# Performance work log

Hardware: AMD Instinct MI355X
Metric: run time of the kernel (lower is better)

The kernel has to match this reference:

```python
import jax, jax.numpy as jnp
import numpy as np
from jax import lax

EPS = 1e-5
K = 13  # correlation window (pad 6 each side)

def _conv(x, w, b):
    # 3x3 conv, stride 1, padding 1, NCHW/OIHW
    y = lax.conv_general_dilated(x, w, (1, 1), ((1, 1), (1, 1)),
                                 dimension_numbers=('NCHW', 'OIHW', 'NCHW'))
    return y + b[None, :, None, None]

def _inorm(x):
    # InstanceNorm2d: per-sample per-channel, biased var, no affine
    m = jnp.mean(x, axis=(2, 3), keepdims=True)
    v = jnp.mean((x - m) ** 2, axis=(2, 3), keepdims=True)
    return (x - m) * lax.rsqrt(v + EPS)

def _block(x, wa, ba, wb, bb):
    x = jax.nn.relu(_conv(x, wa, ba))
    x = jax.nn.relu(_conv(x, wb, bb))
    return _inorm(x)

def _forward(color, corr, w1a, b1a, w1b, b1b, w2a, b2a, w2b, b2b,
             w3a, b3a, w3b, b3b, w4a, b4a, w4b, b4b, H, W):
    conv1 = _block(color[:, :, ::2, ::2], w1a, b1a, w1b, b1b)   # (B,64,2H,2W)
    conv2 = _block(conv1[:, :, ::2, ::2], w2a, b2a, w2b, b2b)   # (B,128,H,W)
    B, C = conv2.shape[0], conv2.shape[1]
    pad = jnp.pad(conv2, ((0, 0), (0, 0), (6, 6), (6, 6)), mode='edge')
    # 'pre' mode: content-adaptive 13x13 windowed weighted sum.
    # accumulating corr[:, t] * shifted-window of conv2_pad.
    def body(acc, t):
        i, j = t // K, t % K
        patch = lax.dynamic_slice(pad, (0, 0, i, j), (B, C, H, W))
        acc = acc + corr[:, t][:, None, :] * patch.reshape(B, C, H * W)
        return acc, None
    align, _ = lax.scan(body, jnp.zeros((B, C, H * W), conv2.dtype),
                        jnp.arange(K * K))
    align_1 = align.reshape(B, C, H, W)                          # (B,128,H,W)
    align_2 = _block(align_1[:, :, ::2, ::2], w3a, b3a, w3b, b3b)  # (B,256,H/2,W/2)
    align_3 = _block(align_2[:, :, ::2, ::2], w4a, b4a, w4b, b4b)  # (B,512,H/4,W/4)
    return (align_1, align_2, align_3)

def setup_inputs() -> dict:
    key = jax.random.key(0)
    ks = jax.random.split(key, 20)
    def w(k, shape):
        return jax.random.normal(k, shape, jnp.float32) * 0.05
    B, H, W = 4, 128, 128
    inp = {
        'color': jax.random.normal(ks[0], (B, 2, 4 * H, 4 * W), jnp.float32),
        'corr': jax.random.normal(ks[1], (B, K * K, H * W), jnp.float32) * 0.05,
        'w1a': w(ks[2], (64, 2, 3, 3)),    'b1a': jnp.zeros((64,), jnp.float32),
        'w1b': w(ks[3], (64, 64, 3, 3)),   'b1b': jnp.zeros((64,), jnp.float32),
        'w2a': w(ks[4], (128, 64, 3, 3)),  'b2a': jnp.zeros((128,), jnp.float32),
        'w2b': w(ks[5], (128, 128, 3, 3)), 'b2b': jnp.zeros((128,), jnp.float32),
        'w3a': w(ks[6], (256, 128, 3, 3)), 'b3a': jnp.zeros((256,), jnp.float32),
        'w3b': w(ks[7], (256, 256, 3, 3)), 'b3b': jnp.zeros((256,), jnp.float32),
        'w4a': w(ks[8], (512, 256, 3, 3)), 'b4a': jnp.zeros((512,), jnp.float32),
        'w4b': w(ks[9], (512, 512, 3, 3)), 'b4b': jnp.zeros((512,), jnp.float32),
        'H': H, 'W': W,
    }
    return inp

def reference(color, corr, w1a, b1a, w1b, b1b, w2a, b2a, w2b, b2b,
              w3a, b3a, w3b, b3b, w4a, b4a, w4b, b4b, H, W):
    return _forward(color, corr, w1a, b1a, w1b, b1b, w2a, b2a, w2b, b2b,
                    w3a, b3a, w3b, b3b, w4a, b4a, w4b, b4b, H, W)
```

## Files before the change

kernel.cpp:

```cpp
#include <hip/hip_runtime.h>
#include <hip/hip_bf16.h>

typedef __hip_bfloat16 bf16;
typedef __attribute__((ext_vector_type(8))) short short8;
typedef __attribute__((ext_vector_type(4))) float f32x4;
typedef __attribute__((address_space(1))) const void gas_void;
typedef __attribute__((address_space(3))) void las_void;

__device__ __forceinline__ float b2f(bf16 v) { return __bfloat162float(v); }
__device__ __forceinline__ bf16 f2b(float v) { return __float2bfloat16(v); }
__device__ __forceinline__ short fbits(float v) {
  bf16 h = f2b(v); return *reinterpret_cast<short*>(&h);
}
__device__ __forceinline__ float sb2f(short s) {
  return b2f(*reinterpret_cast<bf16*>(&s));
}
__device__ __forceinline__ int xcd_swz(int bid, int nwg) {
  int q = nwg >> 3, r = nwg & 7;
  int xcd = bid & 7, idx = bid >> 3;
  return (xcd < r ? xcd * (q + 1) : r * (q + 1) + (xcd - r) * q) + idx;
}

struct RDesc {
  const float* w[7];
  int off8[7];
  int cin[7], cout[7];
  int base[8];
};

__global__ __launch_bounds__(256) void repack_all_k(RDesc d, short* __restrict__ Wr,
                                                    float* __restrict__ zerop)
{
  if (blockIdx.x == 0 && threadIdx.x < 16) zerop[threadIdx.x] = 0.f;
  int blk = blockIdx.x;
  int l = 0;
  while (l < 6 && blk >= d.base[l + 1]) ++l;
  const int Cin = d.cin[l], Cout = d.cout[l];
  const int nkc = Cin >> 5, ncof = Cout >> 4;
  const size_t gid = (size_t)(blk - d.base[l]) * 256 + threadIdx.x;
  const int lane = gid & 63;
  size_t r = gid >> 6;
  const int tap = r % 9; r /= 9;
  const int kcc = r % nkc; r /= nkc;
  const int cof = r % ncof;
  const int hl = r / ncof;
  const float* w = d.w[l];
  const int co = cof * 16 + (lane & 15);
  short8 v;
#pragma unroll
  for (int j = 0; j < 8; ++j) {
    int ci = kcc * 32 + ((lane >> 4) * 8 + j);
    float wv = w[((size_t)co * Cin + ci) * 9 + tap];
    bf16 hi = f2b(wv);
    v[j] = hl ? fbits(wv - b2f(hi)) : *reinterpret_cast<short*>(&hi);
  }
  *reinterpret_cast<short8*>(Wr + ((size_t)d.off8[l] + gid) * 8) = v;
}

template<int R, int CX, int S, int LO, int GL>
__global__ __launch_bounds__(256) void conv_mfma_k(
    const bf16* __restrict__ src, bf16* __restrict__ dst,
    const short8* __restrict__ Wr, const float* __restrict__ bias,
    const float2* __restrict__ stats, float* __restrict__ pout,
    const float* __restrict__ zerop,
    int Win, int Hout, int Wout, int Cin, int Cout, int XT, int KS)
{
  constexpr int ROWS = R + 2;
  constexpr int COLS = CX + 2;
  constexpr int NGR = ROWS * 4 * COLS;
  constexpr int FM = (R * CX) / 32;
  __shared__ short8 a_s[NGR];

  const int ytn = Hout / R;
  const int nxy = XT * ytn;
  const int ncog = Cout >> 6;
  const int wg = xcd_swz(blockIdx.x, gridDim.x);
  const int ks = wg / (ncog * 4 * nxy);
  const int rem2 = wg - ks * (ncog * 4 * nxy);
  const int cog = rem2 / (4 * nxy);
  const int rem = rem2 - cog * (4 * nxy);
  const int b = rem / nxy;
  const int pxb = rem - b * nxy;
  const int xt = pxb % XT, yt = pxb / XT;
  const int x0 = xt * CX, y0 = yt * R;

  const int tid = threadIdx.x, lane = tid & 63, wid = tid >> 6;
  const int wm = wid & 1, wn = wid >> 1;
  const int nkc = Cin >> 5;
  const int nkcs = nkc / KS;
  const int kc0 = ks * nkcs;
  const int ncof = Cout >> 4;
  const int l15 = lane & 15, lg = lane >> 4;

  f32x4 acc[FM][2] = {};

  int arow[FM], acolb[FM];
#pragma unroll
  for (int fm = 0; fm < FM; ++fm) {
    int p = wm * (R * CX / 2) + fm * 16 + l15;
    arow[fm] = p / CX;
    acolb[fm] = p % CX;
  }

  auto bload = [&](int hl, int fn, int kcc, int tap) -> short8 {
    int cof = cog * 4 + wn * 2 + fn;
    return Wr[((((size_t)hl * ncof + cof) * nkc + kcc) * 9 + tap) * 64 + lane];
  };

  short8 bc[2][2], bn_[2][2];
  bc[0][0] = bload(0, 0, kc0, 0); bc[0][1] = bload(0, 1, kc0, 0);
  if (LO) { bc[1][0] = bload(1, 0, kc0, 0); bc[1][1] = bload(1, 1, kc0, 0); }

  for (int kc = kc0; kc < kc0 + nkcs; ++kc) {
    __syncthreads();
    if (GL) {
      for (int s = tid; s < NGR; s += 256) {
        int col = s % COLS, rg = s / COLS;
        int row = rg >> 2, g = rg & 3;
        int sy = y0 + row - 1;
        int sx = x0 + col - 1;
        const short* gp;
        if (sy >= 0 && sy < Hout && sx >= 0 && sx < Wout) {
          int ry = S ? 2 * sy : sy, rx = S ? 2 * sx : sx;
          gp = reinterpret_cast<const short*>(src) +
               (((size_t)b * (S ? 2 * Hout : Hout) + ry) * Win + rx) * Cin +
               kc * 32 + g * 8;
        } else {
          gp = reinterpret_cast<const short*>(zerop);
        }
        __builtin_amdgcn_global_load_lds((gas_void*)gp, (las_void*)&a_s[s], 16, 0, 0);
      }
    } else {
      for (int idx = tid; idx < NGR; idx += 256) {
        int g = idx & 3, cix = idx >> 2;
        int col = cix % COLS, row = cix / COLS;
        int sy = y0 + row - 1;
        int sx = x0 + col - 1;
        short8 v = {};
        if (sy >= 0 && sy < Hout && sx >= 0 && sx < Wout) {
          int ry = S ? 2 * sy : sy, rx = S ? 2 * sx : sx;
          v = *reinterpret_cast<const short8*>(
              reinterpret_cast<const short*>(src) +
              (((size_t)b * (S ? 2 * Hout : Hout) + ry) * Win + rx) * Cin +
              kc * 32 + g * 8);
          if (stats) {
            const float2* st = stats + (size_t)b * Cin + kc * 32 + g * 8;
#pragma unroll
            for (int j = 0; j < 8; ++j)
              v[j] = fbits((sb2f(v[j]) - st[j].x) * st[j].y);
          }
        }
        a_s[(row * 4 + g) * COLS + col] = v;
      }
    }
    __syncthreads();

#pragma unroll
    for (int tap = 0; tap < 9; ++tap) {
      const int dy = tap / 3, dx = tap % 3;
      int nt = tap + 1, nk = kc;
      if (nt == 9) { nt = 0; nk = (kc + 1 < kc0 + nkcs) ? kc + 1 : kc0; }
      bn_[0][0] = bload(0, 0, nk, nt); bn_[0][1] = bload(0, 1, nk, nt);
      if (LO) { bn_[1][0] = bload(1, 0, nk, nt); bn_[1][1] = bload(1, 1, nk, nt); }
      if (LO) {
#pragma unroll
        for (int fm = 0; fm < FM; fm += 2) {
          short8 a0 = a_s[((arow[fm] + dy) * 4 + lg) * COLS + acolb[fm] + dx];
          short8 a1 = a_s[((arow[fm + 1] + dy) * 4 + lg) * COLS + acolb[fm + 1] + dx];
          acc[fm][0]     = __builtin_amdgcn_mfma_f32_16x16x32_bf16(a0, bc[0][0], acc[fm][0], 0, 0, 0);
          acc[fm + 1][0] = __builtin_amdgcn_mfma_f32_16x16x32_bf16(a1, bc[0][0], acc[fm + 1][0], 0, 0, 0);
          acc[fm][1]     = __builtin_amdgcn_mfma_f32_16x16x32_bf16(a0, bc[0][1], acc[fm][1], 0, 0, 0);
          acc[fm + 1][1] = __builtin_amdgcn_mfma_f32_16x16x32_bf16(a1, bc[0][1], acc[fm + 1][1], 0, 0, 0);
          acc[fm][0]     = __builtin_amdgcn_mfma_f32_16x16x32_bf16(a0, bc[1][0], acc[fm][0], 0, 0, 0);
          acc[fm + 1][0] = __builtin_amdgcn_mfma_f32_16x16x32_bf16(a1, bc[1][0], acc[fm + 1][0], 0, 0, 0);
          acc[fm][1]     = __builtin_amdgcn_mfma_f32_16x16x32_bf16(a0, bc[1][1], acc[fm][1], 0, 0, 0);
          acc[fm + 1][1] = __builtin_amdgcn_mfma_f32_16x16x32_bf16(a1, bc[1][1], acc[fm + 1][1], 0, 0, 0);
        }
      } else {
#pragma unroll
        for (int fm = 0; fm < FM; ++fm) {
          short8 a = a_s[((arow[fm] + dy) * 4 + lg) * COLS + acolb[fm] + dx];
          acc[fm][0] = __builtin_amdgcn_mfma_f32_16x16x32_bf16(a, bc[0][0], acc[fm][0], 0, 0, 0);
          acc[fm][1] = __builtin_amdgcn_mfma_f32_16x16x32_bf16(a, bc[0][1], acc[fm][1], 0, 0, 0);
        }
      }
      bc[0][0] = bn_[0][0]; bc[0][1] = bn_[0][1];
      if (LO) { bc[1][0] = bn_[1][0]; bc[1][1] = bn_[1][1]; }
    }
  }

#pragma unroll
  for (int fn = 0; fn < 2; ++fn) {
    int co = cog * 64 + wn * 32 + fn * 16 + l15;
    float bs = bias[co];
#pragma unroll
    for (int fm = 0; fm < FM; ++fm) {
#pragma unroll
      for (int j = 0; j < 4; ++j) {
        int p = wm * (R * CX / 2) + fm * 16 + lg * 4 + j;
        int r = p / CX, x = p % CX;
        size_t oi = ((size_t)(b * Hout + y0 + r) * Wout + x0 + x) * Cout + co;
        if (pout) {
          pout[(size_t)ks * ((size_t)4 * Hout * Wout * Cout) + oi] = acc[fm][fn][j];
        } else {
          dst[oi] = f2b(fmaxf(acc[fm][fn][j] + bs, 0.f));
        }
      }
    }
  }
}

__global__ __launch_bounds__(256) void combine2_k(
    const float* __restrict__ p, const float* __restrict__ bias,
    bf16* __restrict__ dst, int n4, int Cout)
{
  int i = blockIdx.x * 256 + threadIdx.x;
  if (i >= n4) return;
  float4 a = reinterpret_cast<const float4*>(p)[i];
  float4 c = reinterpret_cast<const float4*>(p + (size_t)n4 * 4)[i];
  int co = (i * 4) & (Cout - 1);
  float4 bs = *reinterpret_cast<const float4*>(bias + co);
  short v0 = fbits(fmaxf(a.x + c.x + bs.x, 0.f));
  short v1 = fbits(fmaxf(a.y + c.y + bs.y, 0.f));
  short v2 = fbits(fmaxf(a.z + c.z + bs.z, 0.f));
  short v3 = fbits(fmaxf(a.w + c.w + bs.w, 0.f));
  short4 pk = make_short4(v0, v1, v2, v3);
  *reinterpret_cast<short4*>(reinterpret_cast<short*>(dst) + (size_t)i * 4) = pk;
}

__global__ __launch_bounds__(256) void conv1a_k(
    const float* __restrict__ src, bf16* __restrict__ dst,
    const float* __restrict__ w, const float* __restrict__ bias)
{
  const int b = blockIdx.z, cog = blockIdx.y;
  const int ty0 = (blockIdx.x / 16) * 16, tx0 = (blockIdx.x % 16) * 16;
  const int tid = threadIdx.x, tx = tid & 15, ty = tid >> 4;

  __shared__ float in_s[2][18][18];
  __shared__ __align__(16) float w_s[2][3][3][16];

  for (int idx = tid; idx < 2 * 324; idx += 256) {
    int ci = idx / 324, r = idx - ci * 324;
    int iy = r / 18, ix = r - iy * 18;
    int gy = ty0 + iy - 1, gx = tx0 + ix - 1;
    float v = 0.f;
    if (gy >= 0 && gy < 256 && gx >= 0 && gx < 256)
      v = src[((size_t)(b * 2 + ci) * 512 + 2 * gy) * 512 + 2 * gx];
    in_s[ci][iy][ix] = v;
  }
  for (int idx = tid; idx < 2 * 144; idx += 256) {
    int co = idx & 15, r = idx >> 4;
    int ci = r / 9, k = r - ci * 9;
    w_s[ci][k / 3][k % 3][co] = w[(size_t)((cog * 16 + co) * 2 + ci) * 9 + k];
  }
  __syncthreads();

  float acc[16];
#pragma unroll
  for (int i = 0; i < 16; ++i) acc[i] = 0.f;
  for (int ci = 0; ci < 2; ++ci)
#pragma unroll
    for (int dy = 0; dy < 3; ++dy)
#pragma unroll
      for (int dx = 0; dx < 3; ++dx) {
        float v = in_s[ci][ty + dy][tx + dx];
        const float4* wv = (const float4*)(&w_s[ci][dy][dx][0]);
        float4 w0 = wv[0], w1 = wv[1], w2 = wv[2], w3 = wv[3];
        acc[0] = fmaf(v, w0.x, acc[0]);   acc[1] = fmaf(v, w0.y, acc[1]);
        acc[2] = fmaf(v, w0.z, acc[2]);   acc[3] = fmaf(v, w0.w, acc[3]);
        acc[4] = fmaf(v, w1.x, acc[4]);   acc[5] = fmaf(v, w1.y, acc[5]);
        acc[6] = fmaf(v, w1.z, acc[6]);   acc[7] = fmaf(v, w1.w, acc[7]);
        acc[8] = fmaf(v, w2.x, acc[8]);   acc[9] = fmaf(v, w2.y, acc[9]);
        acc[10] = fmaf(v, w2.z, acc[10]); acc[11] = fmaf(v, w2.w, acc[11]);
        acc[12] = fmaf(v, w3.x, acc[12]); acc[13] = fmaf(v, w3.y, acc[13]);
        acc[14] = fmaf(v, w3.z, acc[14]); acc[15] = fmaf(v, w3.w, acc[15]);
      }

  const int gy = ty0 + ty, gx = tx0 + tx;
  short8 s0, s1;
#pragma unroll
  for (int j = 0; j < 8; ++j) {
    s0[j] = fbits(fmaxf(acc[j] + bias[cog * 16 + j], 0.f));
    s1[j] = fbits(fmaxf(acc[8 + j] + bias[cog * 16 + 8 + j], 0.f));
  }
  short8* dp = reinterpret_cast<short8*>(
      reinterpret_cast<short*>(dst) + (((size_t)(b * 256 + gy) * 256 + gx) * 64 + cog * 16));
  dp[0] = s0; dp[1] = s1;
}

__global__ __launch_bounds__(256) void inorm_stats1_k(
    const bf16* __restrict__ x, float2* __restrict__ part,
    int HW, int C, int nb, int PC)
{
  const int b = blockIdx.y, pc = blockIdx.x;
  const int NC8 = C >> 3;
  const int pgc = 256 / NC8;
  const int c8 = (threadIdx.x % NC8) * 8;
  const int pg = threadIdx.x / NC8;
  const int chunk = HW / PC;
  const int p0 = pc * chunk;

  float s[8] = {}, ss[8] = {};
  for (int p = p0 + pg; p < p0 + chunk; p += pgc) {
    short8 v = *reinterpret_cast<const short8*>(
        reinterpret_cast<const short*>(x) + ((size_t)b * HW + p) * C + c8);
#pragma unroll
    for (int j = 0; j < 8; ++j) {
      float f = sb2f(v[j]);
      s[j] += f; ss[j] += f * f;
    }
  }
  __shared__ float sh[2][2048];
#pragma unroll
  for (int j = 0; j < 8; ++j) {
    sh[0][pg * C + c8 + j] = s[j];
    sh[1][pg * C + c8 + j] = ss[j];
  }
  __syncthreads();
  for (int c = threadIdx.x; c < C; c += 256) {
    float as = 0.f, aq = 0.f;
    for (int g = 0; g < pgc; ++g) { as += sh[0][g * C + c]; aq += sh[1][g * C + c]; }
    part[((size_t)pc * nb + b) * C + c] = make_float2(as, aq);
  }
}

__global__ __launch_bounds__(256) void inorm_stats2_k(
    const float2* __restrict__ part, float2* __restrict__ stats,
    int HW, int C, int PC, int nb)
{
  const int b = blockIdx.y, cg = blockIdx.x;
  const int c = threadIdx.x & 63, i = threadIdx.x >> 6;
  float s = 0.f, ss = 0.f;
  for (int pc = i; pc < PC; pc += 4) {
    float2 v = part[((size_t)pc * nb + b) * C + cg * 64 + c];
    s += v.x; ss += v.y;
  }
  __shared__ float sh[2][4][64];
  sh[0][i][c] = s; sh[1][i][c] = ss;
  __syncthreads();
  if (threadIdx.x < 64) {
    int cc = threadIdx.x;
    float s4 = sh[0][0][cc] + sh[0][1][cc] + sh[0][2][cc] + sh[0][3][cc];
    float q4 = sh[1][0][cc] + sh[1][1][cc] + sh[1][2][cc] + sh[1][3][cc];
    float m = s4 / (float)HW;
    float var = q4 / (float)HW - m * m;
    stats[(size_t)b * C + cg * 64 + cc] = make_float2(m, rsqrtf(var + 1e-5f));
  }
}

__global__ __launch_bounds__(256) void inorm_apply_k(
    const bf16* __restrict__ x, const float2* __restrict__ stats, int HW, int C,
    bf16* __restrict__ dnhwc, float* __restrict__ fnchw)
{
  const int b = blockIdx.z, cg = blockIdx.y;
  const int c = cg * 64 + (threadIdx.x & 63);
  const int p = blockIdx.x * 4 + (threadIdx.x >> 6);
  const float2 st = stats[(size_t)b * C + c];
  const size_t ia = ((size_t)b * HW + p) * C + c;
  const float v = (b2f(x[ia]) - st.x) * st.y;
  if (dnhwc) dnhwc[ia] = f2b(v);
  if (fnchw) fnchw[((size_t)(b * C + c)) * HW + p] = v;
}

__global__ __launch_bounds__(256) void inorm_apply_pad_k(
    const bf16* __restrict__ x, const float2* __restrict__ stats,
    bf16* __restrict__ pad)
{
  const int b = blockIdx.z, cg = blockIdx.y, yy = blockIdx.x;
  const int tid = threadIdx.x;
  __shared__ bf16 t_s[64][130];
  __shared__ float2 st_s[64];
  if (tid < 64) st_s[tid] = stats[(size_t)b * 128 + cg * 64 + tid];
  __syncthreads();

  const int c8 = (tid & 7) * 8, px0 = tid >> 3;
#pragma unroll
  for (int pass = 0; pass < 4; ++pass) {
    int px = pass * 32 + px0;
    short8 v = *reinterpret_cast<const short8*>(
        reinterpret_cast<const short*>(x) +
        ((size_t)(b * 16384 + yy * 128 + px) * 128 + cg * 64 + c8));
#pragma unroll
    for (int j = 0; j < 8; ++j) {
      float2 st = st_s[c8 + j];
      t_s[c8 + j][px] = f2b((sb2f(v[j]) - st.x) * st.y);
    }
  }
  __syncthreads();

  for (int idx = tid; idx < 64 * 18; idx += 256) {
    int c = idx / 18, g = idx - (idx / 18) * 18;
    short8 v;
#pragma unroll
    for (int j = 0; j < 8; ++j) {
      int xx = g * 8 + j - 6;
      xx = xx < 0 ? 0 : (xx > 127 ? 127 : xx);
      v[j] = *reinterpret_cast<short*>(&t_s[c][xx]);
    }
    *reinterpret_cast<short8*>(
        reinterpret_cast<short*>(pad) +
        ((size_t)(b * 128 + cg * 64 + c) * 128 + yy) * 144 + g * 8) = v;
  }
}

__global__ __launch_bounds__(256) void corr_mfma_k(
    const float* __restrict__ corr, const bf16* __restrict__ pad,
    float* __restrict__ outc, bf16* __restrict__ outn, int b0)
{
  __shared__ __align__(16) char smem[26 * 64 * 16];
  short8* a_lds = reinterpret_cast<short8*>(smem);
  float* out_s = reinterpret_cast<float*>(smem);

  const int b = b0 + blockIdx.z;
  const int wg = xcd_swz(blockIdx.x, gridDim.x);
  const int y = wg >> 3, xt = wg & 7;
  const int x0 = xt * 16;
  const int tid = threadIdx.x, lane = tid & 63, wid = tid >> 6;
  const int l15 = lane & 15, lg = lane >> 4;

  for (int idx = tid; idx < 26 * 64; idx += 256) {
    short8 z = {};
    a_lds[idx] = z;
  }
  __syncthreads();

  unsigned short* ah = reinterpret_cast<unsigned short*>(a_lds);
  for (int idx = tid; idx < 169 * 16; idx += 256) {
    int t = idx >> 4, m = idx & 15;
    int dy = t / 13, dx = t - dy * 13;
    float f = corr[((size_t)b * 169 + t) * 16384 + y * 128 + x0 + m];
    bf16 hi = f2b(f);
    unsigned short hb = *reinterpret_cast<unsigned short*>(&hi);
    unsigned short lb = (unsigned short)fbits(f - b2f(hi));
    int k = m + dx;
    int ent = dy * 64 + (k >> 3) * 16 + m;
    ah[ent * 8 + (k & 7)] = hb;
    ah[(13 * 64 + ent) * 8 + (k & 7)] = lb;
  }
  __syncthreads();

  const int cg0 = wid * 2;
  f32x4 a0h = {}, a0l = {}, a1h = {}, a1l = {};
  const short* pb = reinterpret_cast<const short*>(pad);

  for (int dy = 0; dy < 13; ++dy) {
    int rowc = y + dy - 6; rowc = rowc < 0 ? 0 : (rowc > 127 ? 127 : rowc);
    short8 bhi = a_lds[dy * 64 + lane];
    short8 blo = a_lds[(13 + dy) * 64 + lane];
    size_t base0 = ((size_t)(b * 128 + cg0 * 16 + l15) * 128 + rowc) * 144
                   + x0 + lg * 8;
    short8 a0 = *reinterpret_cast<const short8*>(pb + base0);
    short8 a1 = *reinterpret_cast<const short8*>(pb + base0 + (size_t)16 * 128 * 144);
    a0h = __builtin_amdgcn_mfma_f32_16x16x32_bf16(a0, bhi, a0h, 0, 0, 0);
    a1h = __builtin_amdgcn_mfma_f32_16x16x32_bf16(a1, bhi, a1h, 0, 0, 0);
    a0l = __builtin_amdgcn_mfma_f32_16x16x32_bf16(a0, blo, a0l, 0, 0, 0);
    a1l = __builtin_amdgcn_mfma_f32_16x16x32_bf16(a1, blo, a1l, 0, 0, 0);
  }
  f32x4 acc0 = a0h + a0l, acc1 = a1h + a1l;
  __syncthreads();

#pragma unroll
  for (int cgi = 0; cgi < 2; ++cgi) {
    f32x4 a = cgi ? acc1 : acc0;
    float* dst4 = out_s + l15 * 132 + (cg0 + cgi) * 16 + lg * 4;
    *reinterpret_cast<f32x4*>(dst4) = a;
  }
  __syncthreads();

  {
    int px_ = tid >> 4, c8 = (tid & 15) * 8;
    const float* row = out_s + px_ * 132 + c8;
    short8 v;
#pragma unroll
    for (int j = 0; j < 8; ++j) v[j] = fbits(row[j]);
    *reinterpret_cast<short8*>(
        reinterpret_cast<short*>(outn) +
        ((size_t)(b * 16384 + y * 128 + x0 + px_)) * 128 + c8) = v;
  }
  {
    int ch = tid >> 1, pg = tid & 1;
    float v0[4], v1[4];
#pragma unroll
    for (int i = 0; i < 4; ++i) v0[i] = out_s[(pg * 8 + i) * 132 + ch];
#pragma unroll
    for (int i = 0; i < 4; ++i) v1[i] = out_s[(pg * 8 + 4 + i) * 132 + ch];
    float* dst = outc + ((size_t)(b * 128 + ch)) * 16384 + y * 128 + x0 + pg * 8;
    *reinterpret_cast<float4*>(dst) = make_float4(v0[0], v0[1], v0[2], v0[3]);
    *reinterpret_cast<float4*>(dst + 4) = make_float4(v1[0], v1[1], v1[2], v1[3]);
  }
}

extern "C" void kernel_launch(void* const* d_in, const int* in_sizes, int n_in,
                              void* d_out, int out_size, void* d_ws, size_t ws_size,
                              hipStream_t stream) {
  const float* color = (const float*)d_in[0];
  const float* corr  = (const float*)d_in[1];
  const float* w1a = (const float*)d_in[2];  const float* b1a = (const float*)d_in[3];
  const float* w1b = (const float*)d_in[4];  const float* b1b = (const float*)d_in[5];
  const float* w2a = (const float*)d_in[6];  const float* b2a = (const float*)d_in[7];
  const float* w2b = (const float*)d_in[8];  const float* b2b = (const float*)d_in[9];
  const float* w3a = (const float*)d_in[10]; const float* b3a = (const float*)d_in[11];
  const float* w3b = (const float*)d_in[12]; const float* b3b = (const float*)d_in[13];
  const float* w4a = (const float*)d_in[14]; const float* b4a = (const float*)d_in[15];
  const float* w4b = (const float*)d_in[16]; const float* b4b = (const float*)d_in[17];

  float* out = (float*)d_out;
  char* ws = (char*)d_ws;
  const size_t MB = 1048576;
  float2* stats = (float2*)ws;
  short*  WrS   = (short*)(ws + (64 << 10));
  float2* part  = (float2*)(ws + 63 * MB);
  float*  zerop = (float*)(ws + 63 * MB + (800 << 10));
  bf16* P0 = (bf16*)(ws + 10 * MB);
  bf16* P1 = (bf16*)(ws + 27 * MB);
  bf16* P2 = (bf16*)(ws + 44 * MB);
  float* PK = (float*)(ws + 10 * MB);
  bf16* X1 = P0;
  bf16* X2 = (bf16*)d_out;
  const float2* nost = (const float2*)nullptr;
  float* nop = (float*)nullptr;

  RDesc rd;
  rd.w[0] = w1b; rd.w[1] = w2a; rd.w[2] = w2b; rd.w[3] = w3a;
  rd.w[4] = w3b; rd.w[5] = w4a; rd.w[6] = w4b;
  const int off8[7]  = {0, 9216, 27648, 64512, 101376, 175104, 322560};
  const int cin_[7]  = {64, 64, 128, 128, 256, 256, 512};
  const int cout_[7] = {64, 128, 128, 256, 256, 512, 512};
  int bases[8]; bases[0] = 0;
  const int nblk[7] = {36, 72, 144, 144, 288, 576, 1152};
  for (int i = 0; i < 7; ++i) { rd.off8[i] = off8[i]; rd.cin[i] = cin_[i];
    rd.cout[i] = cout_[i]; bases[i + 1] = bases[i] + nblk[i]; }
  for (int i = 0; i < 8; ++i) rd.base[i] = bases[i];
  const short8* WrV = (const short8*)WrS;

  repack_all_k<<<bases[7], 256, 0, stream>>>(rd, WrS, zerop);

  conv1a_k<<<dim3(256, 4, 4), 256, 0, stream>>>(color, X1, w1a, b1a);
  conv_mfma_k<16, 16, 0, 1, 1><<<1024, 256, 0, stream>>>(
      X1, X2, WrV + off8[0], b1b, nost, nop, zerop, 256, 256, 256, 64, 64, 16, 1);
  inorm_stats1_k<<<dim3(64, 4), 256, 0, stream>>>(X2, part, 65536, 64, 4, 64);
  inorm_stats2_k<<<dim3(1, 4), 256, 0, stream>>>(part, stats, 65536, 64, 64, 4);

  conv_mfma_k<16, 16, 1, 1, 0><<<512, 256, 0, stream>>>(
      X2, P0, WrV + off8[1], b2a, stats, nop, zerop, 256, 128, 128, 64, 128, 8, 1);
  conv_mfma_k<16, 16, 0, 1, 1><<<512, 256, 0, stream>>>(
      P0, P1, WrV + off8[2], b2b, nost, nop, zerop, 128, 128, 128, 128, 128, 8, 1);
  inorm_stats1_k<<<dim3(64, 4), 256, 0, stream>>>(P1, part, 16384, 128, 4, 64);
  inorm_stats2_k<<<dim3(2, 4), 256, 0, stream>>>(part, stats, 16384, 128, 64, 4);
  inorm_apply_pad_k<<<dim3(128, 2, 4), 256, 0, stream>>>(P1, stats, P2);

  corr_mfma_k<<<dim3(128 * 8, 1, 4), 256, 0, stream>>>(corr, P2, out, P0, 0);

  conv_mfma_k<8, 16, 1, 0, 1><<<512, 256, 0, stream>>>(
      P0, P1, WrV + off8[3], b3a, nost, nop, zerop, 128, 64, 64, 128, 256, 4, 1);
  conv_mfma_k<8, 16, 0, 0, 1><<<512, 256, 0, stream>>>(
      P1, P2, WrV + off8[4], b3b, nost, nop, zerop, 64, 64, 64, 256, 256, 4, 1);
  inorm_stats1_k<<<dim3(32, 4), 256, 0, stream>>>(P2, part, 4096, 256, 4, 32);
  inorm_stats2_k<<<dim3(4, 4), 256, 0, stream>>>(part, stats, 4096, 256, 32, 4);
  inorm_apply_k<<<dim3(1024, 4, 4), 256, 0, stream>>>(
      P2, stats, 4096, 256, (bf16*)nullptr, out + 8388608);

  conv_mfma_k<4, 16, 1, 0, 0><<<1024, 256, 0, stream>>>(
      P2, (bf16*)nullptr, WrV + off8[5], b4a, stats, PK, zerop, 64, 32, 32, 256, 512, 2, 2);
  combine2_k<<<2048, 256, 0, stream>>>(PK, b4a, P1, 524288, 512);
  conv_mfma_k<4, 16, 0, 0, 1><<<1024, 256, 0, stream>>>(
      P1, (bf16*)nullptr, WrV + off8[6], b4b, nost, PK, zerop, 32, 32, 32, 512, 512, 2, 2);
  combine2_k<<<2048, 256, 0, stream>>>(PK, b4b, P2, 524288, 512);
  inorm_stats1_k<<<dim3(32, 4), 256, 0, stream>>>(P2, part, 1024, 512, 4, 32);
  inorm_stats2_k<<<dim3(8, 4), 256, 0, stream>>>(part, stats, 1024, 512, 32, 4);
  inorm_apply_k<<<dim3(256, 8, 4), 256, 0, stream>>>(
      P2, stats, 1024, 512, (bf16*)nullptr, out + 12582912);
}
```

Before: 416.6 us.

## Reuse LDS rows across vertical taps via register strips; enable split-bf16 for level-3 convs

Adds an ST template mode that reorders the 9 taps column-major. For each horizontal offset it loads one register strip of FM+2 rows from LDS, and the three vertical taps index into that strip instead of issuing separate LDS reads. This cuts LDS read traffic per tap roughly threefold, at the cost of extra registers. The level-3 convs are also switched to LO=1 (hi/lo bf16 weight split), so their weight repack storage doubles and the workspace offsets shift; this adds MFMA work, presumably for accuracy.

Result: slower. 475.1 us (+14.0%).

```diff
diff --git a/kernel.cpp b/kernel.cpp
--- a/kernel.cpp
+++ b/kernel.cpp
@@ -57,7 +57,7 @@
   *reinterpret_cast<short8*>(Wr + ((size_t)d.off8[l] + gid) * 8) = v;
 }
 
-template<int R, int CX, int S, int LO, int GL>
+template<int R, int CX, int S, int LO, int GL, int ST>
 __global__ __launch_bounds__(256) void conv_mfma_k(
     const bf16* __restrict__ src, bf16* __restrict__ dst,
     const short8* __restrict__ Wr, const float* __restrict__ bias,
@@ -69,6 +69,7 @@
   constexpr int COLS = CX + 2;
   constexpr int NGR = ROWS * 4 * COLS;
   constexpr int FM = (R * CX) / 32;
+  static_assert(CX == 16, "strip addressing assumes CX==16");
   __shared__ short8 a_s[NGR];
 
   const int ytn = Hout / R;
@@ -110,6 +111,8 @@
   short8 bc[2][2], bn_[2][2];
   bc[0][0] = bload(0, 0, kc0, 0); bc[0][1] = bload(0, 1, kc0, 0);
   if (LO) { bc[1][0] = bload(1, 0, kc0, 0); bc[1][1] = bload(1, 1, kc0, 0); }
+
+  short8 strip[FM + 2];
 
   for (int kc = kc0; kc < kc0 + nkcs; ++kc) {
     __syncthreads();
@@ -155,37 +158,80 @@
     }
     __syncthreads();
 
-#pragma unroll
-    for (int tap = 0; tap < 9; ++tap) {
-      const int dy = tap / 3, dx = tap % 3;
-      int nt = tap + 1, nk = kc;
-      if (nt == 9) { nt = 0; nk = (kc + 1 < kc0 + nkcs) ? kc + 1 : kc0; }
-      bn_[0][0] = bload(0, 0, nk, nt); bn_[0][1] = bload(0, 1, nk, nt);
-      if (LO) { bn_[1][0] = bload(1, 0, nk, nt); bn_[1][1] = bload(1, 1, nk, nt); }
-      if (LO) {
-#pragma unroll
-        for (int fm = 0; fm < FM; fm += 2) {
-          short8 a0 = a_s[((arow[fm] + dy) * 4 + lg) * COLS + acolb[fm] + dx];
-          short8 a1 = a_s[((arow[fm + 1] + dy) * 4 + lg) * COLS + acolb[fm + 1] + dx];
-          acc[fm][0]     = __builtin_amdgcn_mfma_f32_16x16x32_bf16(a0, bc[0][0], acc[fm][0], 0, 0, 0);
-          acc[fm + 1][0] = __builtin_amdgcn_mfma_f32_16x16x32_bf16(a1, bc[0][0], acc[fm + 1][0], 0, 0, 0);
-          acc[fm][1]     = __builtin_amdgcn_mfma_f32_16x16x32_bf16(a0, bc[0][1], acc[fm][1], 0, 0, 0);
-          acc[fm + 1][1] = __builtin_amdgcn_mfma_f32_16x16x32_bf16(a1, bc[0][1], acc[fm + 1][1], 0, 0, 0);
-          acc[fm][0]     = __builtin_amdgcn_mfma_f32_16x16x32_bf16(a0, bc[1][0], acc[fm][0], 0, 0, 0);
-          acc[fm + 1][0] = __builtin_amdgcn_mfma_f32_16x16x32_bf16(a1, bc[1][0], acc[fm + 1][0], 0, 0, 0);
-          acc[fm][1]     = __builtin_amdgcn_mfma_f32_16x16x32_bf16(a0, bc[1][1], acc[fm][1], 0, 0, 0);
-          acc[fm + 1][1] = __builtin_amdgcn_mfma_f32_16x16x32_bf16(a1, bc[1][1], acc[fm + 1][1], 0, 0, 0);
+    if (ST) {
+#pragma unroll
+      for (int ti = 0; ti < 9; ++ti) {
+        const int dxM = ti / 3, dyM = ti % 3;
+        int tn = ti + 1, nk = kc, ntap;
+        if (tn == 9) { ntap = 0; nk = (kc + 1 < kc0 + nkcs) ? kc + 1 : kc0; }
+        else ntap = (tn % 3) * 3 + (tn / 3);
+        bn_[0][0] = bload(0, 0, nk, ntap); bn_[0][1] = bload(0, 1, nk, ntap);
+        if (LO) { bn_[1][0] = bload(1, 0, nk, ntap); bn_[1][1] = bload(1, 1, nk, ntap); }
+
+        if (dyM == 0) {
+#pragma unroll
+          for (int r = 0; r < FM + 2; ++r)
+            strip[r] = a_s[((wm * FM + r) * 4 + lg) * COLS + l15 + dxM];
         }
-      } else {
-#pragma unroll
-        for (int fm = 0; fm < FM; ++fm) {
-          short8 a = a_s[((arow[fm] + dy) * 4 + lg) * COLS + acolb[fm] + dx];
-          acc[fm][0] = __builtin_amdgcn_mfma_f32_16x16x32_bf16(a, bc[0][0], acc[fm][0], 0, 0, 0);
-          acc[fm][1] = __builtin_amdgcn_mfma_f32_16x16x32_bf16(a, bc[0][1], acc[fm][1], 0, 0, 0);
+
+        if (LO) {
+#pragma unroll
+          for (int fm = 0; fm < FM; fm += 2) {
+            short8 a0 = strip[fm + dyM];
+            short8 a1 = strip[fm + 1 + dyM];
+            acc[fm][0]     = __builtin_amdgcn_mfma_f32_16x16x32_bf16(a0, bc[0][0], acc[fm][0], 0, 0, 0);
+            acc[fm + 1][0] = __builtin_amdgcn_mfma_f32_16x16x32_bf16(a1, bc[0][0], acc[fm + 1][0], 0, 0, 0);
+            acc[fm][1]     = __builtin_amdgcn_mfma_f32_16x16x32_bf16(a0, bc[0][1], acc[fm][1], 0, 0, 0);
+            acc[fm + 1][1] = __builtin_amdgcn_mfma_f32_16x16x32_bf16(a1, bc[0][1], acc[fm + 1][1], 0, 0, 0);
+            acc[fm][0]     = __builtin_amdgcn_mfma_f32_16x16x32_bf16(a0, bc[1][0], acc[fm][0], 0, 0, 0);
+            acc[fm + 1][0] = __builtin_amdgcn_mfma_f32_16x16x32_bf16(a1, bc[1][0], acc[fm + 1][0], 0, 0, 0);
+            acc[fm][1]     = __builtin_amdgcn_mfma_f32_16x16x32_bf16(a0, bc[1][1], acc[fm][1], 0, 0, 0);
+            acc[fm + 1][1] = __builtin_amdgcn_mfma_f32_16x16x32_bf16(a1, bc[1][1], acc[fm + 1][1], 0, 0, 0);
+          }
+        } else {
+#pragma unroll
+          for (int fm = 0; fm < FM; ++fm) {
+            short8 a = strip[fm + dyM];
+            acc[fm][0] = __builtin_amdgcn_mfma_f32_16x16x32_bf16(a, bc[0][0], acc[fm][0], 0, 0, 0);
+            acc[fm][1] = __builtin_amdgcn_mfma_f32_16x16x32_bf16(a, bc[0][1], acc[fm][1], 0, 0, 0);
+          }
         }
+        bc[0][0] = bn_[0][0]; bc[0][1] = bn_[0][1];
+        if (LO) { bc[1][0] = bn_[1][0]; bc[1][1] = bn_[1][1]; }
       }
-      bc[0][0] = bn_[0][0]; bc[0][1] = bn_[0][1];
-      if (LO) { bc[1][0] = bn_[1][0]; bc[1][1] = bn_[1][1]; }
+    } else {
+#pragma unroll
+      for (int tap = 0; tap < 9; ++tap) {
+        const int dy = tap / 3, dx = tap % 3;
+        int nt = tap + 1, nk = kc;
+        if (nt == 9) { nt = 0; nk = (kc + 1 < kc0 + nkcs) ? kc + 1 : kc0; }
+        bn_[0][0] = bload(0, 0, nk, nt); bn_[0][1] = bload(0, 1, nk, nt);
+        if (LO) { bn_[1][0] = bload(1, 0, nk, nt); bn_[1][1] = bload(1, 1, nk, nt); }
+        if (LO) {
+#pragma unroll
+          for (int fm = 0; fm < FM; fm += 2) {
+            short8 a0 = a_s[((arow[fm] + dy) * 4 + lg) * COLS + acolb[fm] + dx];
+            short8 a1 = a_s[((arow[fm + 1] + dy) * 4 + lg) * COLS + acolb[fm + 1] + dx];
+            acc[fm][0]     = __builtin_amdgcn_mfma_f32_16x16x32_bf16(a0, bc[0][0], acc[fm][0], 0, 0, 0);
+            acc[fm + 1][0] = __builtin_amdgcn_mfma_f32_16x16x32_bf16(a1, bc[0][0], acc[fm + 1][0], 0, 0, 0);
+            acc[fm][1]     = __builtin_amdgcn_mfma_f32_16x16x32_bf16(a0, bc[0][1], acc[fm][1], 0, 0, 0);
+            acc[fm + 1][1] = __builtin_amdgcn_mfma_f32_16x16x32_bf16(a1, bc[0][1], acc[fm + 1][1], 0, 0, 0);
+            acc[fm][0]     = __builtin_amdgcn_mfma_f32_16x16x32_bf16(a0, bc[1][0], acc[fm][0], 0, 0, 0);
+            acc[fm + 1][0] = __builtin_amdgcn_mfma_f32_16x16x32_bf16(a1, bc[1][0], acc[fm + 1][0], 0, 0, 0);
+            acc[fm][1]     = __builtin_amdgcn_mfma_f32_16x16x32_bf16(a0, bc[1][1], acc[fm][1], 0, 0, 0);
+            acc[fm + 1][1] = __builtin_amdgcn_mfma_f32_16x16x32_bf16(a1, bc[1][1], acc[fm + 1][1], 0, 0, 0);
+          }
+        } else {
+#pragma unroll
+          for (int fm = 0; fm < FM; ++fm) {
+            short8 a = a_s[((arow[fm] + dy) * 4 + lg) * COLS + acolb[fm] + dx];
+            acc[fm][0] = __builtin_amdgcn_mfma_f32_16x16x32_bf16(a, bc[0][0], acc[fm][0], 0, 0, 0);
+            acc[fm][1] = __builtin_amdgcn_mfma_f32_16x16x32_bf16(a, bc[0][1], acc[fm][1], 0, 0, 0);
+          }
+        }
+        bc[0][0] = bn_[0][0]; bc[0][1] = bn_[0][1];
+        if (LO) { bc[1][0] = bn_[1][0]; bc[1][1] = bn_[1][1]; }
+      }
     }
   }
 
@@ -509,13 +555,13 @@
   const size_t MB = 1048576;
   float2* stats = (float2*)ws;
   short*  WrS   = (short*)(ws + (64 << 10));
-  float2* part  = (float2*)(ws + 63 * MB);
-  float*  zerop = (float*)(ws + 63 * MB + (800 << 10));
-  bf16* P0 = (bf16*)(ws + 10 * MB);
-  bf16* P1 = (bf16*)(ws + 27 * MB);
-  bf16* P2 = (bf16*)(ws + 44 * MB);
-  float* PK = (float*)(ws + 10 * MB);
-  bf16* X1 = P0;
+  float*  zerop = (float*)(ws + 11 * MB + (512 << 10));
+  float2* part  = (float2*)(ws + 11 * MB + (768 << 10));
+  bf16* P0 = (bf16*)(ws + 12 * MB);
+  bf16* P1 = (bf16*)(ws + 29 * MB);
+  bf16* P2 = (bf16*)(ws + 46 * MB);
+  float* PK = (float*)(ws + 12 * MB);
+  bf16* X1 = (bf16*)(ws + 29 * MB);
   bf16* X2 = (bf16*)d_out;
   const float2* nost = (const float2*)nullptr;
   float* nop = (float*)nullptr;
@@ -523,11 +569,11 @@
   RDesc rd;
   rd.w[0] = w1b; rd.w[1] = w2a; rd.w[2] = w2b; rd.w[3] = w3a;
   rd.w[4] = w3b; rd.w[5] = w4a; rd.w[6] = w4b;
-  const int off8[7]  = {0, 9216, 27648, 64512, 101376, 175104, 322560};
+  const int off8[7]  = {0, 9216, 27648, 64512, 138240, 285696, 433152};
   const int cin_[7]  = {64, 64, 128, 128, 256, 256, 512};
   const int cout_[7] = {64, 128, 128, 256, 256, 512, 512};
   int bases[8]; bases[0] = 0;
-  const int nblk[7] = {36, 72, 144, 144, 288, 576, 1152};
+  const int nblk[7] = {36, 72, 144, 288, 576, 576, 1152};
   for (int i = 0; i < 7; ++i) { rd.off8[i] = off8[i]; rd.cin[i] = cin_[i];
     rd.cout[i] = cout_[i]; bases[i + 1] = bases[i] + nblk[i]; }
   for (int i = 0; i < 8; ++i) rd.base[i] = bases[i];
@@ -536,14 +582,14 @@
   repack_all_k<<<bases[7], 256, 0, stream>>>(rd, WrS, zerop);
 
   conv1a_k<<<dim3(256, 4, 4), 256, 0, stream>>>(color, X1, w1a, b1a);
-  conv_mfma_k<16, 16, 0, 1, 1><<<1024, 256, 0, stream>>>(
+  conv_mfma_k<16, 16, 0, 1, 1, 1><<<1024, 256, 0, stream>>>(
       X1, X2, WrV + off8[0], b1b, nost, nop, zerop, 256, 256, 256, 64, 64, 16, 1);
   inorm_stats1_k<<<dim3(64, 4), 256, 0, stream>>>(X2, part, 65536, 64, 4, 64);
   inorm_stats2_k<<<dim3(1, 4), 256, 0, stream>>>(part, stats, 65536, 64, 64, 4);
 
-  conv_mfma_k<16, 16, 1, 1, 0><<<512, 256, 0, stream>>>(
+  conv_mfma_k<16, 16, 1, 1, 0, 1><<<512, 256, 0, stream>>>(
       X2, P0, WrV + off8[1], b2a, stats, nop, zerop, 256, 128, 128, 64, 128, 8, 1);
-  conv_mfma_k<16, 16, 0, 1, 1><<<512, 256, 0, stream>>>(
+  conv_mfma_k<16, 16, 0, 1, 1, 1><<<512, 256, 0, stream>>>(
       P0, P1, WrV + off8[2], b2b, nost, nop, zerop, 128, 128, 128, 128, 128, 8, 1);
   inorm_stats1_k<<<dim3(64, 4), 256, 0, stream>>>(P1, part, 16384, 128, 4, 64);
   inorm_stats2_k<<<dim3(2, 4), 256, 0, stream>>>(part, stats, 16384, 128, 64, 4);
@@ -551,19 +597,19 @@
 
   corr_mfma_k<<<dim3(128 * 8, 1, 4), 256, 0, stream>>>(corr, P2, out, P0, 0);
 
-  conv_mfma_k<8, 16, 1, 0, 1><<<512, 256, 0, stream>>>(
+  conv_mfma_k<8, 16, 1, 1, 1, 1><<<512, 256, 0, stream>>>(
       P0, P1, WrV + off8[3], b3a, nost, nop, zerop, 128, 64, 64, 128, 256, 4, 1);
-  conv_mfma_k<8, 16, 0, 0, 1><<<512, 256, 0, stream>>>(
+  conv_mfma_k<8, 16, 0, 1, 1, 1><<<512, 256, 0, stream>>>(
       P1, P2, WrV + off8[4], b3b, nost, nop, zerop, 64, 64, 64, 256, 256, 4, 1);
   inorm_stats1_k<<<dim3(32, 4), 256, 0, stream>>>(P2, part, 4096, 256, 4, 32);
   inorm_stats2_k<<<dim3(4, 4), 256, 0, stream>>>(part, stats, 4096, 256, 32, 4);
   inorm_apply_k<<<dim3(1024, 4, 4), 256, 0, stream>>>(
       P2, stats, 4096, 256, (bf16*)nullptr, out + 8388608);
 
-  conv_mfma_k<4, 16, 1, 0, 0><<<1024, 256, 0, stream>>>(
+  conv_mfma_k<4, 16, 1, 0, 0, 0><<<1024, 256, 0, stream>>>(
       P2, (bf16*)nullptr, WrV + off8[5], b4a, stats, PK, zerop, 64, 32, 32, 256, 512, 2, 2);
   combine2_k<<<2048, 256, 0, stream>>>(PK, b4a, P1, 524288, 512);
-  conv_mfma_k<4, 16, 0, 0, 1><<<1024, 256, 0, stream>>>(
+  conv_mfma_k<4, 16, 0, 0, 1, 0><<<1024, 256, 0, stream>>>(
       P1, (bf16*)nullptr, WrV + off8[6], b4b, nost, PK, zerop, 32, 32, 32, 512, 512, 2, 2);
   combine2_k<<<2048, 256, 0, stream>>>(PK, b4b, P2, 524288, 512);
   inorm_stats1_k<<<dim3(32, 4), 256, 0, stream>>>(P2, part, 1024, 512, 4, 32);
```
